# Kernel optimization log

Measured on AMD Instinct MI355X. Metric: run time of the kernel, lower is better.

The kernel has to match this reference:

```python
import jax, jax.numpy as jnp
import numpy as np

EPS = 1e-7  # keras.backend.epsilon()


def setup_inputs() -> dict:
    key = jax.random.key(0)
    k1, k2 = jax.random.split(key)
    B, S, D = 8, 1024, 768
    # scale down: module exponentiates raw dot products with no max-subtraction
    input_a = jax.random.normal(k1, (B, S, D), dtype=jnp.float32) * 0.05
    input_mask = jax.random.randint(k2, (B, S), 0, 2, dtype=jnp.int32)
    return {"input_a": input_a, "input_mask": input_mask}


def reference(input_a, input_mask):
    # e = exp(Q K^T) with Q = K = input_a, attend_type='dot' (no scaling)
    e = jnp.exp(jnp.einsum('bsd,btd->bst', input_a, input_a))  # [B,S,S]
    m = input_mask.astype(input_a.dtype)
    e = e * m[:, :, None] * m[:, None, :]  # mask rows and cols
    e = e / (jnp.sum(e, axis=-1, keepdims=True) + EPS)  # renormalize
    attend = jnp.einsum('bst,btd->bsd', e, input_a)  # V = input_a
    return attend
```

## Files before the change

kernel.cpp:

```cpp
#include <hip/hip_runtime.h>
#include <cstdint>
#include <cstddef>

#define BATCH 8
#define SEQ 1024
#define DIM 768
#define EPS_K 1e-7f

typedef __bf16 bf16x8 __attribute__((ext_vector_type(8)));
typedef float f32x4 __attribute__((ext_vector_type(4)));
typedef uint16_t u16x8 __attribute__((ext_vector_type(8)));

__device__ __forceinline__ uint16_t f2bf(float f) {
  union { float f; uint32_t u; } v; v.f = f;
  uint32_t u = v.u;
  u += 0x7FFFu + ((u >> 16) & 1u);
  return (uint16_t)(u >> 16);
}

__device__ __forceinline__ void gload16(const void* g, void* l) {
  __builtin_amdgcn_global_load_lds(
      (const __attribute__((address_space(1))) uint32_t*)g,
      (__attribute__((address_space(3))) uint32_t*)l, 16, 0, 0);
}

__global__ __launch_bounds__(256) void convert_kernel(const float* __restrict__ A,
                                                      uint16_t* __restrict__ ab,
                                                      uint16_t* __restrict__ at) {
  const int b  = blockIdx.z;
  const int s0 = blockIdx.y * 64;
  const int d0 = blockIdx.x * 64;
  __shared__ uint16_t tl[64][80];
  const int tid = threadIdx.x;

#pragma unroll
  for (int i = 0; i < 2; ++i) {
    const int sl = (tid >> 3) + i * 32;
    const int ch = tid & 7;
    const float* src = A + ((size_t)b * SEQ + s0 + sl) * DIM + d0 + ch * 8;
    float4 f0 = *(const float4*)src;
    float4 f1 = *(const float4*)(src + 4);
    u16x8 h;
    h[0] = f2bf(f0.x); h[1] = f2bf(f0.y); h[2] = f2bf(f0.z); h[3] = f2bf(f0.w);
    h[4] = f2bf(f1.x); h[5] = f2bf(f1.y); h[6] = f2bf(f1.z); h[7] = f2bf(f1.w);
    *(u16x8*)&ab[((size_t)b * SEQ + s0 + sl) * DIM + d0 + ch * 8] = h;
    *(u16x8*)&tl[sl][ch * 8] = h;
  }
  __syncthreads();
  const int dl = tid >> 2;
#pragma unroll
  for (int i = 0; i < 2; ++i) {
    const int sc = (tid & 3) + i * 4;
    u16x8 h;
#pragma unroll
    for (int e = 0; e < 8; ++e) h[e] = tl[sc * 8 + e][dl];
    *(u16x8*)&at[((size_t)b * DIM + d0 + dl) * SEQ + s0 + sc * 8] = h;
  }
}


__global__ __launch_bounds__(512, 2) void scores_kernel(const uint16_t* __restrict__ ab,
                                                        const int* __restrict__ mask,
                                                        uint16_t* __restrict__ P) {
  const int b    = blockIdx.x & 7;
  const int tile = blockIdx.x >> 3;
  const int s0   = (tile >> 3) * 256;
  const int t0   = (tile & 7) * 128;

  const int tid  = threadIdx.x;
  const int lane = tid & 63;
  const int wid  = tid >> 6;
  const int wr   = wid >> 1;
  const int wc   = wid & 1;

  __shared__ __align__(16) uint16_t lA[2][256 * 64];
  __shared__ __align__(16) uint16_t lB[2][128 * 64];

  const uint16_t* gA = ab + ((size_t)b * SEQ + s0) * DIM;
  const uint16_t* gB = ab + ((size_t)b * SEQ + t0) * DIM;

  const int srl  = tid >> 3;
  const int schx = ((tid & 7) ^ (srl & 7)) << 3;
  const int sdst = srl * 64 + (tid & 7) * 8;

#define STAGE(buf, k0)                                                         \
  do {                                                                         \
    _Pragma("unroll")                                                          \
    for (int _i = 0; _i < 4; ++_i)                                             \
      gload16(gA + (size_t)(srl + _i * 64) * DIM + (k0) + schx,                \
              &lA[buf][sdst + _i * 64 * 64]);                                  \
    _Pragma("unroll")                                                          \
    for (int _i = 0; _i < 2; ++_i)                                             \
      gload16(gB + (size_t)(srl + _i * 64) * DIM + (k0) + schx,                \
              &lB[buf][sdst + _i * 64 * 64]);                                  \
  } while (0)

  f32x4 acc[4][4];
#pragma unroll
  for (int m = 0; m < 4; ++m)
#pragma unroll
    for (int n = 0; n < 4; ++n) acc[m][n] = f32x4{0.f, 0.f, 0.f, 0.f};

  const int rA  = wr * 64 + (lane & 15);
  const int rB  = wc * 64 + (lane & 15);
  const int cx0 = (((lane >> 4) + 0) ^ (lane & 7)) << 3;
  const int cx1 = (((lane >> 4) + 4) ^ (lane & 7)) << 3;

  STAGE(0, 0);
  int cur = 0;
  for (int t = 0; t < DIM / 64; ++t) {
    if (t + 1 < DIM / 64) {
      STAGE(cur ^ 1, (t + 1) * 64);
      asm volatile("s_waitcnt vmcnt(6)" ::: "memory");
    } else {
      asm volatile("s_waitcnt vmcnt(0)" ::: "memory");
    }
    __builtin_amdgcn_s_barrier();

    bf16x8 bfr[2][4];
#pragma unroll
    for (int n = 0; n < 4; ++n) {
      bfr[0][n] = *(const bf16x8*)&lB[cur][(rB + n * 16) * 64 + cx0];
      bfr[1][n] = *(const bf16x8*)&lB[cur][(rB + n * 16) * 64 + cx1];
    }
    __builtin_amdgcn_s_setprio(1);
#pragma unroll
    for (int m = 0; m < 4; ++m) {
      bf16x8 a0 = *(const bf16x8*)&lA[cur][(rA + m * 16) * 64 + cx0];
      bf16x8 a1 = *(const bf16x8*)&lA[cur][(rA + m * 16) * 64 + cx1];
#pragma unroll
      for (int n = 0; n < 4; ++n) {
        acc[m][n] = __builtin_amdgcn_mfma_f32_16x16x32_bf16(a0, bfr[0][n], acc[m][n], 0, 0, 0);
        acc[m][n] = __builtin_amdgcn_mfma_f32_16x16x32_bf16(a1, bfr[1][n], acc[m][n], 0, 0, 0);
      }
    }
    __builtin_amdgcn_s_setprio(0);
    __builtin_amdgcn_s_barrier();
    cur ^= 1;
  }
#undef STAGE

  const int* mk = mask + b * SEQ;
  uint16_t* Pb = P + (size_t)b * SEQ * SEQ;
  float mc[4];
#pragma unroll
  for (int n = 0; n < 4; ++n) mc[n] = (float)mk[t0 + wc * 64 + n * 16 + (lane & 15)];
#pragma unroll
  for (int m = 0; m < 4; ++m) {
#pragma unroll
    for (int j = 0; j < 4; ++j) {
      const int rs = s0 + wr * 64 + m * 16 + (lane >> 4) * 4 + j;
      const float mr = (float)mk[rs];
#pragma unroll
      for (int n = 0; n < 4; ++n) {
        const int ct = t0 + wc * 64 + n * 16 + (lane & 15);
        float e = __expf(acc[m][n][j]) * mr * mc[n];
        Pb[(size_t)rs * SEQ + ct] = f2bf(e);
      }
    }
  }
}

__global__ __launch_bounds__(512, 2) void out_kernel(const uint16_t* __restrict__ P,
                                                     const uint16_t* __restrict__ at,
                                                     float* __restrict__ out) {
  const int b    = blockIdx.x & 7;
  const int tile = blockIdx.x >> 3;
  const int q0   = (tile / 6) * 256;
  const int d0   = (tile % 6) * 128;

  const int tid  = threadIdx.x;
  const int lane = tid & 63;
  const int wid  = tid >> 6;
  const int wr   = wid >> 1;
  const int wc   = wid & 1;

  __shared__ __align__(16) uint16_t lA[2][256 * 64];
  __shared__ __align__(16) uint16_t lB[2][128 * 64];

  const uint16_t* gA = P  + ((size_t)b * SEQ + q0) * SEQ;
  const uint16_t* gB = at + ((size_t)b * DIM + d0) * SEQ;

  const int srl  = tid >> 3;
  const int schx = ((tid & 7) ^ (srl & 7)) << 3;
  const int sdst = srl * 64 + (tid & 7) * 8;

#define STAGE(buf, k0)                                                         \
  do {                                                                         \
    _Pragma("unroll")                                                          \
    for (int _i = 0; _i < 4; ++_i)                                             \
      gload16(gA + (size_t)(srl + _i * 64) * SEQ + (k0) + schx,                \
              &lA[buf][sdst + _i * 64 * 64]);                                  \
    _Pragma("unroll")                                                          \
    for (int _i = 0; _i < 2; ++_i)                                             \
      gload16(gB + (size_t)(srl + _i * 64) * SEQ + (k0) + schx,                \
              &lB[buf][sdst + _i * 64 * 64]);                                  \
  } while (0)

  f32x4 acc[4][4];
  f32x4 accd[4];
#pragma unroll
  for (int m = 0; m < 4; ++m) {
    accd[m] = f32x4{0.f, 0.f, 0.f, 0.f};
#pragma unroll
    for (int n = 0; n < 4; ++n) acc[m][n] = f32x4{0.f, 0.f, 0.f, 0.f};
  }
  bf16x8 ones;
#pragma unroll
  for (int i = 0; i < 8; ++i) ones[i] = (__bf16)1.0f;

  const int rA  = wr * 64 + (lane & 15);
  const int rB  = wc * 64 + (lane & 15);
  const int cx0 = (((lane >> 4) + 0) ^ (lane & 7)) << 3;
  const int cx1 = (((lane >> 4) + 4) ^ (lane & 7)) << 3;

  STAGE(0, 0);
  int cur = 0;
  for (int t = 0; t < SEQ / 64; ++t) {
    if (t + 1 < SEQ / 64) {
      STAGE(cur ^ 1, (t + 1) * 64);
      asm volatile("s_waitcnt vmcnt(6)" ::: "memory");
    } else {
      asm volatile("s_waitcnt vmcnt(0)" ::: "memory");
    }
    __builtin_amdgcn_s_barrier();

    bf16x8 bfr[2][4];
#pragma unroll
    for (int n = 0; n < 4; ++n) {
      bfr[0][n] = *(const bf16x8*)&lB[cur][(rB + n * 16) * 64 + cx0];
      bfr[1][n] = *(const bf16x8*)&lB[cur][(rB + n * 16) * 64 + cx1];
    }
    __builtin_amdgcn_s_setprio(1);
#pragma unroll
    for (int m = 0; m < 4; ++m) {
      bf16x8 a0 = *(const bf16x8*)&lA[cur][(rA + m * 16) * 64 + cx0];
      bf16x8 a1 = *(const bf16x8*)&lA[cur][(rA + m * 16) * 64 + cx1];
#pragma unroll
      for (int n = 0; n < 4; ++n) {
        acc[m][n] = __builtin_amdgcn_mfma_f32_16x16x32_bf16(a0, bfr[0][n], acc[m][n], 0, 0, 0);
        acc[m][n] = __builtin_amdgcn_mfma_f32_16x16x32_bf16(a1, bfr[1][n], acc[m][n], 0, 0, 0);
      }
      accd[m] = __builtin_amdgcn_mfma_f32_16x16x32_bf16(a0, ones, accd[m], 0, 0, 0);
      accd[m] = __builtin_amdgcn_mfma_f32_16x16x32_bf16(a1, ones, accd[m], 0, 0, 0);
    }
    __builtin_amdgcn_s_setprio(0);
    __builtin_amdgcn_s_barrier();
    cur ^= 1;
  }
#undef STAGE

  float* ob = out + (size_t)b * SEQ * DIM;
#pragma unroll
  for (int m = 0; m < 4; ++m) {
#pragma unroll
    for (int j = 0; j < 4; ++j) {
      const int q  = q0 + wr * 64 + m * 16 + (lane >> 4) * 4 + j;
      const float sc = 1.0f / (accd[m][j] + EPS_K);
#pragma unroll
      for (int n = 0; n < 4; ++n) {
        const int d = d0 + wc * 64 + n * 16 + (lane & 15);
        ob[(size_t)q * DIM + d] = acc[m][n][j] * sc;
      }
    }
  }
}

extern "C" void kernel_launch(void* const* d_in, const int* in_sizes, int n_in,
                              void* d_out, int out_size, void* d_ws, size_t ws_size,
                              hipStream_t stream) {
  (void)in_sizes; (void)n_in; (void)out_size; (void)ws_size;
  const float* A    = (const float*)d_in[0];
  const int*   mask = (const int*)d_in[1];
  float*       out  = (float*)d_out;

  char* ws = (char*)d_ws;
  const size_t NB_AB = (size_t)BATCH * SEQ * DIM * 2;
  const size_t NB_AT = NB_AB;
  uint16_t* ab = (uint16_t*)(ws);
  uint16_t* at = (uint16_t*)(ws + NB_AB);
  uint16_t* P  = (uint16_t*)(ws + NB_AB + NB_AT);

  convert_kernel<<<dim3(DIM / 64, SEQ / 64, BATCH), dim3(256), 0, stream>>>(A, ab, at);
  scores_kernel<<<dim3(32 * BATCH), dim3(512), 0, stream>>>(ab, mask, P);
  out_kernel<<<dim3(24 * BATCH), dim3(512), 0, stream>>>(P, at, out);
}
```

Measured before the change: 124.5 us.

## Interleave global prefetch with MFMA phases in both GEMM main loops

Both GEMM K-loops are split into four sub-phases, each separated by a barrier. Each sub-phase loads only part of the B and A fragments from LDS and issues only a slice of the next tile's global-to-LDS loads, so memory traffic is spread across the compute instead of issued in one burst. The wait count now only requires the previous tile's loads to have landed, and fewer fragment registers are live at once. The cost is twice as many workgroup barriers per K-step, which could stall waves.

Measured after the change: 127.9 us. +2.7%, slower.

```diff
diff --git a/kernel.cpp b/kernel.cpp
--- a/kernel.cpp
+++ b/kernel.cpp
@@ -10,6 +10,8 @@
 typedef __bf16 bf16x8 __attribute__((ext_vector_type(8)));
 typedef float f32x4 __attribute__((ext_vector_type(4)));
 typedef uint16_t u16x8 __attribute__((ext_vector_type(8)));
+
+#define MFMA(a, b, c) __builtin_amdgcn_mfma_f32_16x16x32_bf16((a), (b), (c), 0, 0, 0)
 
 __device__ __forceinline__ uint16_t f2bf(float f) {
   union { float f; uint32_t u; } v; v.f = f;
@@ -32,7 +34,6 @@
   const int d0 = blockIdx.x * 64;
   __shared__ uint16_t tl[64][80];
   const int tid = threadIdx.x;
-
 #pragma unroll
   for (int i = 0; i < 2; ++i) {
     const int sl = (tid >> 3) + i * 32;
@@ -83,17 +84,14 @@
   const int schx = ((tid & 7) ^ (srl & 7)) << 3;
   const int sdst = srl * 64 + (tid & 7) * 8;
 
-#define STAGE(buf, k0)                                                         \
-  do {                                                                         \
-    _Pragma("unroll")                                                          \
-    for (int _i = 0; _i < 4; ++_i)                                             \
-      gload16(gA + (size_t)(srl + _i * 64) * DIM + (k0) + schx,                \
-              &lA[buf][sdst + _i * 64 * 64]);                                  \
-    _Pragma("unroll")                                                          \
-    for (int _i = 0; _i < 2; ++_i)                                             \
-      gload16(gB + (size_t)(srl + _i * 64) * DIM + (k0) + schx,                \
-              &lB[buf][sdst + _i * 64 * 64]);                                  \
-  } while (0)
+#define STAGE_A2(buf, k0, h)                                                   \
+  { gload16(gA + (size_t)(srl + (2*(h)) * 64) * DIM + (k0) + schx,             \
+            &lA[buf][sdst + (2*(h)) * 4096]);                                  \
+    gload16(gA + (size_t)(srl + (2*(h)+1) * 64) * DIM + (k0) + schx,           \
+            &lA[buf][sdst + (2*(h)+1) * 4096]); }
+#define STAGE_B1(buf, k0, h)                                                   \
+  gload16(gB + (size_t)(srl + (h) * 64) * DIM + (k0) + schx,                   \
+          &lB[buf][sdst + (h) * 4096]);
 
   f32x4 acc[4][4];
 #pragma unroll
@@ -106,39 +104,58 @@
   const int cx0 = (((lane >> 4) + 0) ^ (lane & 7)) << 3;
   const int cx1 = (((lane >> 4) + 4) ^ (lane & 7)) << 3;
 
-  STAGE(0, 0);
+  STAGE_A2(0, 0, 0); STAGE_A2(0, 0, 1); STAGE_B1(0, 0, 0); STAGE_B1(0, 0, 1);
+
+  const int NT = DIM / 64;
   int cur = 0;
-  for (int t = 0; t < DIM / 64; ++t) {
-    if (t + 1 < DIM / 64) {
-      STAGE(cur ^ 1, (t + 1) * 64);
-      asm volatile("s_waitcnt vmcnt(6)" ::: "memory");
-    } else {
-      asm volatile("s_waitcnt vmcnt(0)" ::: "memory");
-    }
-    __builtin_amdgcn_s_barrier();
-
-    bf16x8 bfr[2][4];
-#pragma unroll
-    for (int n = 0; n < 4; ++n) {
-      bfr[0][n] = *(const bf16x8*)&lB[cur][(rB + n * 16) * 64 + cx0];
-      bfr[1][n] = *(const bf16x8*)&lB[cur][(rB + n * 16) * 64 + cx1];
-    }
-    __builtin_amdgcn_s_setprio(1);
-#pragma unroll
-    for (int m = 0; m < 4; ++m) {
-      bf16x8 a0 = *(const bf16x8*)&lA[cur][(rA + m * 16) * 64 + cx0];
-      bf16x8 a1 = *(const bf16x8*)&lA[cur][(rA + m * 16) * 64 + cx1];
-#pragma unroll
-      for (int n = 0; n < 4; ++n) {
-        acc[m][n] = __builtin_amdgcn_mfma_f32_16x16x32_bf16(a0, bfr[0][n], acc[m][n], 0, 0, 0);
-        acc[m][n] = __builtin_amdgcn_mfma_f32_16x16x32_bf16(a1, bfr[1][n], acc[m][n], 0, 0, 0);
-      }
-    }
+  for (int t = 0; t < NT; ++t) {
+    const int k0n = (t + 1) * 64;
+    const bool pf = (t + 1 < NT);
+    const int nx = cur ^ 1;
+    if (pf) { STAGE_A2(nx, k0n, 0); asm volatile("s_waitcnt vmcnt(2)" ::: "memory"); }
+    else    {                        asm volatile("s_waitcnt vmcnt(0)" ::: "memory"); }
+    __builtin_amdgcn_s_barrier();
+
+    bf16x8 bq[4], alo, ahi;
+#pragma unroll
+    for (int n = 0; n < 4; ++n) bq[n] = *(const bf16x8*)&lB[cur][(rB + n * 16) * 64 + cx0];
+    alo = *(const bf16x8*)&lA[cur][(rA + 0) * 64 + cx0];
+    ahi = *(const bf16x8*)&lA[cur][(rA + 16) * 64 + cx0];
+    if (pf) STAGE_A2(nx, k0n, 1);
+    __builtin_amdgcn_s_setprio(1);
+#pragma unroll
+    for (int n = 0; n < 4; ++n) { acc[0][n] = MFMA(alo, bq[n], acc[0][n]); acc[1][n] = MFMA(ahi, bq[n], acc[1][n]); }
+    __builtin_amdgcn_s_setprio(0);
+    __builtin_amdgcn_s_barrier();
+    alo = *(const bf16x8*)&lA[cur][(rA + 32) * 64 + cx0];
+    ahi = *(const bf16x8*)&lA[cur][(rA + 48) * 64 + cx0];
+    if (pf) STAGE_B1(nx, k0n, 0);
+    __builtin_amdgcn_s_setprio(1);
+#pragma unroll
+    for (int n = 0; n < 4; ++n) { acc[2][n] = MFMA(alo, bq[n], acc[2][n]); acc[3][n] = MFMA(ahi, bq[n], acc[3][n]); }
+    __builtin_amdgcn_s_setprio(0);
+    __builtin_amdgcn_s_barrier();
+#pragma unroll
+    for (int n = 0; n < 4; ++n) bq[n] = *(const bf16x8*)&lB[cur][(rB + n * 16) * 64 + cx1];
+    alo = *(const bf16x8*)&lA[cur][(rA + 0) * 64 + cx1];
+    ahi = *(const bf16x8*)&lA[cur][(rA + 16) * 64 + cx1];
+    if (pf) STAGE_B1(nx, k0n, 1);
+    __builtin_amdgcn_s_setprio(1);
+#pragma unroll
+    for (int n = 0; n < 4; ++n) { acc[0][n] = MFMA(alo, bq[n], acc[0][n]); acc[1][n] = MFMA(ahi, bq[n], acc[1][n]); }
+    __builtin_amdgcn_s_setprio(0);
+    __builtin_amdgcn_s_barrier();
+    alo = *(const bf16x8*)&lA[cur][(rA + 32) * 64 + cx1];
+    ahi = *(const bf16x8*)&lA[cur][(rA + 48) * 64 + cx1];
+    __builtin_amdgcn_s_setprio(1);
+#pragma unroll
+    for (int n = 0; n < 4; ++n) { acc[2][n] = MFMA(alo, bq[n], acc[2][n]); acc[3][n] = MFMA(ahi, bq[n], acc[3][n]); }
     __builtin_amdgcn_s_setprio(0);
     __builtin_amdgcn_s_barrier();
     cur ^= 1;
   }
-#undef STAGE
+#undef STAGE_A2
+#undef STAGE_B1
 
   const int* mk = mask + b * SEQ;
   uint16_t* Pb = P + (size_t)b * SEQ * SEQ;
@@ -185,17 +202,14 @@
   const int schx = ((tid & 7) ^ (srl & 7)) << 3;
   const int sdst = srl * 64 + (tid & 7) * 8;
 
-#define STAGE(buf, k0)                                                         \
-  do {                                                                         \
-    _Pragma("unroll")                                                          \
-    for (int _i = 0; _i < 4; ++_i)                                             \
-      gload16(gA + (size_t)(srl + _i * 64) * SEQ + (k0) + schx,                \
-              &lA[buf][sdst + _i * 64 * 64]);                                  \
-    _Pragma("unroll")                                                          \
-    for (int _i = 0; _i < 2; ++_i)                                             \
-      gload16(gB + (size_t)(srl + _i * 64) * SEQ + (k0) + schx,                \
-              &lB[buf][sdst + _i * 64 * 64]);                                  \
-  } while (0)
+#define STAGE_A2(buf, k0, h)                                                   \
+  { gload16(gA + (size_t)(srl + (2*(h)) * 64) * SEQ + (k0) + schx,             \
+            &lA[buf][sdst + (2*(h)) * 4096]);                                  \
+    gload16(gA + (size_t)(srl + (2*(h)+1) * 64) * SEQ + (k0) + schx,           \
+            &lA[buf][sdst + (2*(h)+1) * 4096]); }
+#define STAGE_B1(buf, k0, h)                                                   \
+  gload16(gB + (size_t)(srl + (h) * 64) * SEQ + (k0) + schx,                   \
+          &lB[buf][sdst + (h) * 4096]);
 
   f32x4 acc[4][4];
   f32x4 accd[4];
@@ -214,41 +228,62 @@
   const int cx0 = (((lane >> 4) + 0) ^ (lane & 7)) << 3;
   const int cx1 = (((lane >> 4) + 4) ^ (lane & 7)) << 3;
 
-  STAGE(0, 0);
+  STAGE_A2(0, 0, 0); STAGE_A2(0, 0, 1); STAGE_B1(0, 0, 0); STAGE_B1(0, 0, 1);
+
+  const int NT = SEQ / 64;
   int cur = 0;
-  for (int t = 0; t < SEQ / 64; ++t) {
-    if (t + 1 < SEQ / 64) {
-      STAGE(cur ^ 1, (t + 1) * 64);
-      asm volatile("s_waitcnt vmcnt(6)" ::: "memory");
-    } else {
-      asm volatile("s_waitcnt vmcnt(0)" ::: "memory");
-    }
-    __builtin_amdgcn_s_barrier();
-
-    bf16x8 bfr[2][4];
-#pragma unroll
-    for (int n = 0; n < 4; ++n) {
-      bfr[0][n] = *(const bf16x8*)&lB[cur][(rB + n * 16) * 64 + cx0];
-      bfr[1][n] = *(const bf16x8*)&lB[cur][(rB + n * 16) * 64 + cx1];
-    }
-    __builtin_amdgcn_s_setprio(1);
-#pragma unroll
-    for (int m = 0; m < 4; ++m) {
-      bf16x8 a0 = *(const bf16x8*)&lA[cur][(rA + m * 16) * 64 + cx0];
-      bf16x8 a1 = *(const bf16x8*)&lA[cur][(rA + m * 16) * 64 + cx1];
-#pragma unroll
-      for (int n = 0; n < 4; ++n) {
-        acc[m][n] = __builtin_amdgcn_mfma_f32_16x16x32_bf16(a0, bfr[0][n], acc[m][n], 0, 0, 0);
-        acc[m][n] = __builtin_amdgcn_mfma_f32_16x16x32_bf16(a1, bfr[1][n], acc[m][n], 0, 0, 0);
-      }
-      accd[m] = __builtin_amdgcn_mfma_f32_16x16x32_bf16(a0, ones, accd[m], 0, 0, 0);
-      accd[m] = __builtin_amdgcn_mfma_f32_16x16x32_bf16(a1, ones, accd[m], 0, 0, 0);
-    }
+  for (int t = 0; t < NT; ++t) {
+    const int k0n = (t + 1) * 64;
+    const bool pf = (t + 1 < NT);
+    const int nx = cur ^ 1;
+    if (pf) { STAGE_A2(nx, k0n, 0); asm volatile("s_waitcnt vmcnt(2)" ::: "memory"); }
+    else    {                        asm volatile("s_waitcnt vmcnt(0)" ::: "memory"); }
+    __builtin_amdgcn_s_barrier();
+
+    bf16x8 bq[4], alo, ahi;
+#pragma unroll
+    for (int n = 0; n < 4; ++n) bq[n] = *(const bf16x8*)&lB[cur][(rB + n * 16) * 64 + cx0];
+    alo = *(const bf16x8*)&lA[cur][(rA + 0) * 64 + cx0];
+    ahi = *(const bf16x8*)&lA[cur][(rA + 16) * 64 + cx0];
+    if (pf) STAGE_A2(nx, k0n, 1);
+    __builtin_amdgcn_s_setprio(1);
+#pragma unroll
+    for (int n = 0; n < 4; ++n) { acc[0][n] = MFMA(alo, bq[n], acc[0][n]); acc[1][n] = MFMA(ahi, bq[n], acc[1][n]); }
+    accd[0] = MFMA(alo, ones, accd[0]); accd[1] = MFMA(ahi, ones, accd[1]);
+    __builtin_amdgcn_s_setprio(0);
+    __builtin_amdgcn_s_barrier();
+    alo = *(const bf16x8*)&lA[cur][(rA + 32) * 64 + cx0];
+    ahi = *(const bf16x8*)&lA[cur][(rA + 48) * 64 + cx0];
+    if (pf) STAGE_B1(nx, k0n, 0);
+    __builtin_amdgcn_s_setprio(1);
+#pragma unroll
+    for (int n = 0; n < 4; ++n) { acc[2][n] = MFMA(alo, bq[n], acc[2][n]); acc[3][n] = MFMA(ahi, bq[n], acc[3][n]); }
+    accd[2] = MFMA(alo, ones, accd[2]); accd[3] = MFMA(ahi, ones, accd[3]);
+    __builtin_amdgcn_s_setprio(0);
+    __builtin_amdgcn_s_barrier();
+#pragma unroll
+    for (int n = 0; n < 4; ++n) bq[n] = *(const bf16x8*)&lB[cur][(rB + n * 16) * 64 + cx1];
+    alo = *(const bf16x8*)&lA[cur][(rA + 0) * 64 + cx1];
+    ahi = *(const bf16x8*)&lA[cur][(rA + 16) * 64 + cx1];
+    if (pf) STAGE_B1(nx, k0n, 1);
+    __builtin_amdgcn_s_setprio(1);
+#pragma unroll
+    for (int n = 0; n < 4; ++n) { acc[0][n] = MFMA(alo, bq[n], acc[0][n]); acc[1][n] = MFMA(ahi, bq[n], acc[1][n]); }
+    accd[0] = MFMA(alo, ones, accd[0]); accd[1] = MFMA(ahi, ones, accd[1]);
+    __builtin_amdgcn_s_setprio(0);
+    __builtin_amdgcn_s_barrier();
+    alo = *(const bf16x8*)&lA[cur][(rA + 32) * 64 + cx1];
+    ahi = *(const bf16x8*)&lA[cur][(rA + 48) * 64 + cx1];
+    __builtin_amdgcn_s_setprio(1);
+#pragma unroll
+    for (int n = 0; n < 4; ++n) { acc[2][n] = MFMA(alo, bq[n], acc[2][n]); acc[3][n] = MFMA(ahi, bq[n], acc[3][n]); }
+    accd[2] = MFMA(alo, ones, accd[2]); accd[3] = MFMA(ahi, ones, accd[3]);
     __builtin_amdgcn_s_setprio(0);
     __builtin_amdgcn_s_barrier();
     cur ^= 1;
   }
-#undef STAGE
+#undef STAGE_A2
+#undef STAGE_B1
 
   float* ob = out + (size_t)b * SEQ * DIM;
 #pragma unroll
```
